# Kernel optimization log

Hardware: AMD Instinct MI355X
Metric: run time of the kernel (lower is better)

The kernel has to match this reference:

```python
import jax, jax.numpy as jnp
import numpy as np

B, D_IN, D_OUT = 16384, 1024, 1024


def setup_inputs() -> dict:
    key = jax.random.key(0)
    ks = jax.random.split(key, 14)
    s_x = 1.0 / np.sqrt(D_IN)
    s_h = 1.0 / np.sqrt(D_OUT)
    inp = {
        "inputs": jax.random.normal(ks[0], (B, D_IN), dtype=jnp.float32),
        "hist": jax.random.normal(ks[1], (B, D_OUT), dtype=jnp.float32),
        "carousel": 1,
    }
    names = ["f", "i", "o", "c"]
    for g, n in enumerate(names):
        inp[f"W{n}x"] = jax.random.normal(ks[2 + 3 * g], (D_IN, D_OUT), dtype=jnp.float32) * s_x
        inp[f"W{n}h"] = jax.random.normal(ks[3 + 3 * g], (D_OUT, D_OUT), dtype=jnp.float32) * s_h
        inp[f"b{n}"] = jnp.zeros((D_OUT,), dtype=jnp.float32)
    return inp


def reference(inputs, hist, carousel, Wfx, Wfh, bf, Wix, Wih, bi, Wox, Woh, bo, Wcx, Wch, bc):
    # Each GateMirrored: act(x @ Wx + h @ Wh + b)
    def gate(Wx, Wh, b, act):
        return act(inputs @ Wx + hist @ Wh + b)

    f = gate(Wfx, Wfh, bf, jax.nn.sigmoid)
    i = gate(Wix, Wih, bi, jax.nn.sigmoid)
    o = gate(Wox, Woh, bo, jax.nn.sigmoid)
    g = gate(Wcx, Wch, bc, jnp.tanh)

    c = f * jnp.float32(carousel) + i * g
    h = o * c
    return (h, c)
```

## Files before the change

### kernel.cpp

```cpp
#include <hip/hip_runtime.h>
#include <stdint.h>
#include <stddef.h>

#define B_ROWS 16384
#define DIN 1024
#define DOUT 1024
#define KDIM 2048

#define BM 256
#define BNP 256
#define BK 64

typedef __bf16 bf16x8 __attribute__((ext_vector_type(8)));
typedef float floatx4 __attribute__((ext_vector_type(4)));

__device__ __forceinline__ unsigned short f2bf(float f) {
  unsigned int u = __float_as_uint(f);
  u += 0x7fffu + ((u >> 16) & 1u);
  return (unsigned short)(u >> 16);
}

__device__ __forceinline__ void async16(const void* g, void* l) {
  __builtin_amdgcn_global_load_lds(
      (__attribute__((address_space(1))) void*)(g),
      (__attribute__((address_space(3))) void*)(l), 16, 0, 0);
}

__device__ __forceinline__ float sigmoid_f(float x) {
  return 1.0f / (1.0f + __expf(-x));
}
__device__ __forceinline__ float tanh_f(float x) {
  return 2.0f / (1.0f + __expf(-2.0f * x)) - 1.0f;
}

__global__ void prep_kernel(
    const float* __restrict__ inp, const float* __restrict__ hist,
    const float* __restrict__ s0, const float* __restrict__ s1,
    const float* __restrict__ s2, const float* __restrict__ s3,
    const float* __restrict__ s4, const float* __restrict__ s5,
    const float* __restrict__ s6, const float* __restrict__ s7,
    unsigned short* __restrict__ xb, unsigned short* __restrict__ wt) {
  __shared__ float tile[32][33];
  const int tid = threadIdx.x;
  if (blockIdx.x < 32768) {
    int idx = blockIdx.x * 256 + tid;
    const int per = B_ROWS * DIN / 4;
    const float* src;
    int colOff;
    int i = idx;
    if (i < per) { src = inp; colOff = 0; }
    else         { src = hist; colOff = DIN; i -= per; }
    int e = i * 4;
    int row = e >> 10;
    int col = e & 1023;
    const float4 v = *(const float4*)(src + (size_t)row * 1024 + col);
    ushort4 o;
    o.x = f2bf(v.x); o.y = f2bf(v.y); o.z = f2bf(v.z); o.w = f2bf(v.w);
    *(ushort4*)(xb + (size_t)row * KDIM + colOff + col) = o;
    return;
  }
  const int bb = blockIdx.x - 32768;
  const int bx = bb & 31, by = (bb >> 5) & 31, z = bb >> 10;
  const float* src;
  switch (z) {
    case 0: src = s0; break; case 1: src = s1; break;
    case 2: src = s2; break; case 3: src = s3; break;
    case 4: src = s4; break; case 5: src = s5; break;
    case 6: src = s6; break; default: src = s7; break;
  }
  const int g = z >> 1, part = z & 1;
  const int tx = tid & 31, ty = tid >> 5;
  const int n0 = bx * 32, k0 = by * 32;
#pragma unroll
  for (int j = 0; j < 32; j += 8)
    tile[ty + j][tx] = src[(size_t)(k0 + ty + j) * DOUT + n0 + tx];
  __syncthreads();
#pragma unroll
  for (int j = 0; j < 32; j += 8) {
    const int n = n0 + ty + j;
    const int np = ((n >> 4) << 6) + g * 16 + (n & 15);
    wt[(size_t)np * KDIM + part * DIN + k0 + tx] = f2bf(tile[tx][ty + j]);
  }
}

#define FENCE() __builtin_amdgcn_sched_barrier(0)
#define BAR() do { FENCE(); __builtin_amdgcn_s_barrier(); FENCE(); } while (0)
#define WAITV(N) asm volatile("s_waitcnt vmcnt(" #N ")" ::: "memory")
#define REGOFF(BUF, KH) (((BUF) * 2 + (KH)) << 13)

#define STAGE_A(BUF, KH, KT) do {                                          \
    unsigned short* d_ = As + REGOFF(BUF, KH) + tid * 8;                   \
    async16(agA + (KT) + (KH) * 32, d_);                                   \
    async16(agA + 128 * KDIM + (KT) + (KH) * 32, d_ + 4096);               \
  } while (0)
#define STAGE_B(BUF, KH, KT) do {                                          \
    unsigned short* d_ = Bs + REGOFF(BUF, KH) + tid * 8;                   \
    async16(agB + (KT) + (KH) * 32, d_);                                   \
    async16(agB + 128 * KDIM + (KT) + (KH) * 32, d_ + 4096);               \
  } while (0)
#define LDA4(BUF, KK, MH) do {                                             \
    const unsigned short* b_ = As + REGOFF(BUF, KK) + (MH) * 2048 + aoff;  \
    _Pragma("unroll")                                                      \
    for (int mi = 0; mi < 4; ++mi)                                         \
      av[mi] = *(const bf16x8*)(b_ + mi * 512);                            \
  } while (0)
#define LDB4(BUF, KK) do {                                                 \
    const unsigned short* b_ = Bs + REGOFF(BUF, KK) + boff;                \
    _Pragma("unroll")                                                      \
    for (int ni = 0; ni < 4; ++ni)                                         \
      bv[ni] = *(const bf16x8*)(b_ + ni * 512);                            \
  } while (0)
#define MFMA16(MH) do {                                                    \
    __builtin_amdgcn_s_setprio(1);                                         \
    _Pragma("unroll")                                                      \
    for (int mi = 0; mi < 4; ++mi)                                         \
      _Pragma("unroll")                                                    \
      for (int ni = 0; ni < 4; ++ni)                                       \
        acc[(MH) * 4 + mi][ni] = __builtin_amdgcn_mfma_f32_16x16x32_bf16(  \
            av[mi], bv[ni], acc[(MH) * 4 + mi][ni], 0, 0, 0);              \
    __builtin_amdgcn_s_setprio(0);                                         \
  } while (0)

__global__ __launch_bounds__(512, 2) void lstm_fused_kernel(
    const unsigned short* __restrict__ Xb,
    const unsigned short* __restrict__ Wt2,
    const float* __restrict__ b_f, const float* __restrict__ b_i,
    const float* __restrict__ b_o, const float* __restrict__ b_c,
    const int* __restrict__ carousel,
    float* __restrict__ out) {
  __shared__ unsigned short As[4 * 256 * 32];
  __shared__ unsigned short Bs[4 * 256 * 32];

  const int tid  = threadIdx.x;
  const int lane = tid & 63;
  const int wave = tid >> 6;
  const int wr   = wave >> 2;
  const int wc   = wave & 3;
  const int m16  = lane & 15;
  const int quad = lane >> 4;
  const int ua   = quad ^ ((m16 >> 1) & 3);
  const int bm   = blockIdx.y * BM;
  const int cg   = blockIdx.x;

  const unsigned short* Wp = Wt2 + (size_t)cg * BNP * KDIM;

  const int col = cg * 64 + wc * 16 + m16;
  const float bfv = b_f[col], biv = b_i[col], bov = b_o[col], bcv = b_c[col];
  const float cf  = (float)carousel[0];
  FENCE();

  const int srow   = tid >> 2;
  const int schunk = (tid & 3) ^ ((srow >> 1) & 3);
  const unsigned short* agA = Xb + (size_t)(bm + srow) * KDIM + schunk * 8;
  const unsigned short* agB = Wp + (size_t)srow * KDIM + schunk * 8;

  const int aoff = (wr * 128 + m16) * 32 + ua * 8;
  const int boff = (wc * 64 + m16) * 32 + ua * 8;

  floatx4 acc[8][4];
#pragma unroll
  for (int mi = 0; mi < 8; ++mi)
#pragma unroll
    for (int ni = 0; ni < 4; ++ni)
      acc[mi][ni] = (floatx4){0.f, 0.f, 0.f, 0.f};

  bf16x8 av[4], bv[4];

  STAGE_B(0, 0, 0);
  STAGE_A(0, 0, 0);
  STAGE_B(0, 1, 0);
  STAGE_A(0, 1, 0);
  STAGE_B(1, 0, 64);
  STAGE_A(1, 0, 64);
  STAGE_B(1, 1, 64);
  WAITV(10);
  BAR();

#pragma unroll 1
  for (int p = 0; p < 15; ++p) {
    const int kt = p * 128;
    LDA4(0, 0, 0); LDB4(0, 0);
    STAGE_A(1, 1, kt + 64);
    BAR(); MFMA16(0); BAR();
    LDA4(0, 0, 1);
    STAGE_B(0, 0, kt + 128);
    WAITV(10); BAR(); MFMA16(1); BAR();
    LDA4(0, 1, 0); LDB4(0, 1);
    STAGE_A(0, 0, kt + 128);
    BAR(); MFMA16(0); BAR();
    LDA4(0, 1, 1);
    STAGE_B(0, 1, kt + 128);
    WAITV(10); BAR(); MFMA16(1); BAR();
    LDA4(1, 0, 0); LDB4(1, 0);
    STAGE_A(0, 1, kt + 128);
    BAR(); MFMA16(0); BAR();
    LDA4(1, 0, 1);
    STAGE_B(1, 0, kt + 192);
    WAITV(10); BAR(); MFMA16(1); BAR();
    LDA4(1, 1, 0); LDB4(1, 1);
    STAGE_A(1, 0, kt + 192);
    BAR(); MFMA16(0); BAR();
    LDA4(1, 1, 1);
    STAGE_B(1, 1, kt + 192);
    WAITV(10); BAR(); MFMA16(1); BAR();
  }

  LDA4(0, 0, 0); LDB4(0, 0);
  STAGE_A(1, 1, 1984);
  BAR(); MFMA16(0); BAR();
  LDA4(0, 0, 1);
  WAITV(8); BAR(); MFMA16(1); BAR();
  LDA4(0, 1, 0); LDB4(0, 1);
  BAR(); MFMA16(0); BAR();
  LDA4(0, 1, 1);
  WAITV(4); BAR(); MFMA16(1); BAR();
  LDA4(1, 0, 0); LDB4(1, 0);
  BAR(); MFMA16(0); BAR();
  LDA4(1, 0, 1);
  WAITV(0); BAR(); MFMA16(1); BAR();
  LDA4(1, 1, 0); LDB4(1, 1);
  MFMA16(0);
  LDA4(1, 1, 1);
  MFMA16(1);

  const int rbase = bm + wr * 128 + quad * 4;
#pragma unroll
  for (int mi = 0; mi < 8; ++mi) {
#pragma unroll
    for (int r = 0; r < 4; ++r) {
      const int row = rbase + mi * 16 + r;
      const float f = sigmoid_f(acc[mi][0][r] + bfv);
      const float i = sigmoid_f(acc[mi][1][r] + biv);
      const float o = sigmoid_f(acc[mi][2][r] + bov);
      const float g = tanh_f   (acc[mi][3][r] + bcv);
      const float c = f * cf + i * g;
      const float h = o * c;
      out[(size_t)row * DOUT + col] = h;
      out[(size_t)(B_ROWS * DOUT) + (size_t)row * DOUT + col] = c;
    }
  }
}

extern "C" void kernel_launch(void* const* d_in, const int* in_sizes, int n_in,
                              void* d_out, int out_size, void* d_ws, size_t ws_size,
                              hipStream_t stream) {
  const float* inputs = (const float*)d_in[0];
  const float* hist   = (const float*)d_in[1];
  const int* carousel = (const int*)d_in[2];
  const float* Wfx = (const float*)d_in[3];
  const float* Wfh = (const float*)d_in[4];
  const float* bfv = (const float*)d_in[5];
  const float* Wix = (const float*)d_in[6];
  const float* Wih = (const float*)d_in[7];
  const float* biv = (const float*)d_in[8];
  const float* Wox = (const float*)d_in[9];
  const float* Woh = (const float*)d_in[10];
  const float* bov = (const float*)d_in[11];
  const float* Wcx = (const float*)d_in[12];
  const float* Wch = (const float*)d_in[13];
  const float* bcv = (const float*)d_in[14];

  unsigned short* Xb  = (unsigned short*)d_ws;
  unsigned short* Wt2 = Xb + (size_t)B_ROWS * KDIM;

  prep_kernel<<<40960, 256, 0, stream>>>(
      inputs, hist, Wfx, Wfh, Wix, Wih, Wox, Woh, Wcx, Wch, Xb, Wt2);

  dim3 grid(16, B_ROWS / BM);
  lstm_fused_kernel<<<grid, 512, 0, stream>>>(
      Xb, Wt2, bfv, biv, bov, bcv, carousel, (float*)d_out);
}
```

Baseline: 520.6 us.

## Restructure GEMM main loop to load full A fragment and issue 32 MFMAs per barrier phase

The main loop now stages A and B tiles together in one macro and loads all eight A fragments per k-half instead of splitting each k-half into two half-M phases. Each k-half issues 32 MFMAs between a single pair of barriers, halving the barrier count. Global pointers are advanced incrementally rather than recomputed from the loop index. The cost is more VGPRs for the A fragments, which may pressure the two-blocks-per-CU occupancy target, and less interleaving of LDS reads with MFMA work.

```diff
diff --git a/kernel.cpp b/kernel.cpp
--- a/kernel.cpp
+++ b/kernel.cpp
@@ -88,37 +88,36 @@
 #define WAITV(N) asm volatile("s_waitcnt vmcnt(" #N ")" ::: "memory")
 #define REGOFF(BUF, KH) (((BUF) * 2 + (KH)) << 13)
 
-#define STAGE_A(BUF, KH, KT) do {                                          \
-    unsigned short* d_ = As + REGOFF(BUF, KH) + tid * 8;                   \
-    async16(agA + (KT) + (KH) * 32, d_);                                   \
-    async16(agA + 128 * KDIM + (KT) + (KH) * 32, d_ + 4096);               \
-  } while (0)
-#define STAGE_B(BUF, KH, KT) do {                                          \
-    unsigned short* d_ = Bs + REGOFF(BUF, KH) + tid * 8;                   \
-    async16(agB + (KT) + (KH) * 32, d_);                                   \
-    async16(agB + 128 * KDIM + (KT) + (KH) * 32, d_ + 4096);               \
-  } while (0)
-#define LDA4(BUF, KK, MH) do {                                             \
-    const unsigned short* b_ = As + REGOFF(BUF, KK) + (MH) * 2048 + aoff;  \
-    _Pragma("unroll")                                                      \
-    for (int mi = 0; mi < 4; ++mi)                                         \
-      av[mi] = *(const bf16x8*)(b_ + mi * 512);                            \
-  } while (0)
-#define LDB4(BUF, KK) do {                                                 \
-    const unsigned short* b_ = Bs + REGOFF(BUF, KK) + boff;                \
-    _Pragma("unroll")                                                      \
-    for (int ni = 0; ni < 4; ++ni)                                         \
-      bv[ni] = *(const bf16x8*)(b_ + ni * 512);                            \
-  } while (0)
-#define MFMA16(MH) do {                                                    \
-    __builtin_amdgcn_s_setprio(1);                                         \
-    _Pragma("unroll")                                                      \
-    for (int mi = 0; mi < 4; ++mi)                                         \
-      _Pragma("unroll")                                                    \
-      for (int ni = 0; ni < 4; ++ni)                                       \
-        acc[(MH) * 4 + mi][ni] = __builtin_amdgcn_mfma_f32_16x16x32_bf16(  \
-            av[mi], bv[ni], acc[(MH) * 4 + mi][ni], 0, 0, 0);              \
-    __builtin_amdgcn_s_setprio(0);                                         \
+#define STAGE(BUF, KH, OFFE) do {                                           \
+    unsigned short* dA_ = As + REGOFF(BUF, KH) + tid * 8;                   \
+    unsigned short* dB_ = Bs + REGOFF(BUF, KH) + tid * 8;                   \
+    async16(pA0 + (OFFE), dA_);                                             \
+    async16(pA1 + (OFFE), dA_ + 4096);                                      \
+    async16(pB0 + (OFFE), dB_);                                             \
+    async16(pB1 + (OFFE), dB_ + 4096);                                      \
+  } while (0)
+
+#define LDB4(BUF, KK) do {                                                  \
+    const unsigned short* b_ = Bs + REGOFF(BUF, KK) + boff;                 \
+    _Pragma("unroll")                                                       \
+    for (int ni = 0; ni < 4; ++ni)                                          \
+      bv[ni] = *(const bf16x8*)(b_ + ni * 512);                             \
+  } while (0)
+#define LDA8(BUF, KK) do {                                                  \
+    const unsigned short* a_ = As + REGOFF(BUF, KK) + aoff;                 \
+    _Pragma("unroll")                                                       \
+    for (int mi = 0; mi < 8; ++mi)                                          \
+      av[mi] = *(const bf16x8*)(a_ + mi * 512);                             \
+  } while (0)
+#define MFMA32() do {                                                       \
+    __builtin_amdgcn_s_setprio(1);                                          \
+    _Pragma("unroll")                                                       \
+    for (int mi = 0; mi < 8; ++mi)                                          \
+      _Pragma("unroll")                                                     \
+      for (int ni = 0; ni < 4; ++ni)                                        \
+        acc[mi][ni] = __builtin_amdgcn_mfma_f32_16x16x32_bf16(              \
+            av[mi], bv[ni], acc[mi][ni], 0, 0, 0);                          \
+    __builtin_amdgcn_s_setprio(0);                                          \
   } while (0)
 
 __global__ __launch_bounds__(512, 2) void lstm_fused_kernel(
@@ -151,8 +150,10 @@
 
   const int srow   = tid >> 2;
   const int schunk = (tid & 3) ^ ((srow >> 1) & 3);
-  const unsigned short* agA = Xb + (size_t)(bm + srow) * KDIM + schunk * 8;
-  const unsigned short* agB = Wp + (size_t)srow * KDIM + schunk * 8;
+  const unsigned short* pA0 = Xb + (size_t)(bm + srow) * KDIM + schunk * 8;
+  const unsigned short* pA1 = pA0 + (size_t)128 * KDIM;
+  const unsigned short* pB0 = Wp + (size_t)srow * KDIM + schunk * 8;
+  const unsigned short* pB1 = pB0 + (size_t)128 * KDIM;
 
   const int aoff = (wr * 128 + m16) * 32 + ua * 8;
   const int boff = (wc * 64 + m16) * 32 + ua * 8;
@@ -164,64 +165,54 @@
     for (int ni = 0; ni < 4; ++ni)
       acc[mi][ni] = (floatx4){0.f, 0.f, 0.f, 0.f};
 
-  bf16x8 av[4], bv[4];
-
-  STAGE_B(0, 0, 0);
-  STAGE_A(0, 0, 0);
-  STAGE_B(0, 1, 0);
-  STAGE_A(0, 1, 0);
-  STAGE_B(1, 0, 64);
-  STAGE_A(1, 0, 64);
-  STAGE_B(1, 1, 64);
-  WAITV(10);
+  bf16x8 av[8], bv[4];
+
+  STAGE(0, 0, 0);
+  STAGE(0, 1, 32);
+  STAGE(1, 0, 64);
+  WAITV(8);
   BAR();
 
 #pragma unroll 1
   for (int p = 0; p < 15; ++p) {
-    const int kt = p * 128;
-    LDA4(0, 0, 0); LDB4(0, 0);
-    STAGE_A(1, 1, kt + 64);
-    BAR(); MFMA16(0); BAR();
-    LDA4(0, 0, 1);
-    STAGE_B(0, 0, kt + 128);
-    WAITV(10); BAR(); MFMA16(1); BAR();
-    LDA4(0, 1, 0); LDB4(0, 1);
-    STAGE_A(0, 0, kt + 128);
-    BAR(); MFMA16(0); BAR();
-    LDA4(0, 1, 1);
-    STAGE_B(0, 1, kt + 128);
-    WAITV(10); BAR(); MFMA16(1); BAR();
-    LDA4(1, 0, 0); LDB4(1, 0);
-    STAGE_A(0, 1, kt + 128);
-    BAR(); MFMA16(0); BAR();
-    LDA4(1, 0, 1);
-    STAGE_B(1, 0, kt + 192);
-    WAITV(10); BAR(); MFMA16(1); BAR();
-    LDA4(1, 1, 0); LDB4(1, 1);
-    STAGE_A(1, 0, kt + 192);
-    BAR(); MFMA16(0); BAR();
-    LDA4(1, 1, 1);
-    STAGE_B(1, 1, kt + 192);
-    WAITV(10); BAR(); MFMA16(1); BAR();
-  }
-
-  LDA4(0, 0, 0); LDB4(0, 0);
-  STAGE_A(1, 1, 1984);
-  BAR(); MFMA16(0); BAR();
-  LDA4(0, 0, 1);
-  WAITV(8); BAR(); MFMA16(1); BAR();
-  LDA4(0, 1, 0); LDB4(0, 1);
-  BAR(); MFMA16(0); BAR();
-  LDA4(0, 1, 1);
-  WAITV(4); BAR(); MFMA16(1); BAR();
-  LDA4(1, 0, 0); LDB4(1, 0);
-  BAR(); MFMA16(0); BAR();
-  LDA4(1, 0, 1);
-  WAITV(0); BAR(); MFMA16(1); BAR();
-  LDA4(1, 1, 0); LDB4(1, 1);
-  MFMA16(0);
-  LDA4(1, 1, 1);
-  MFMA16(1);
+    LDB4(0, 0); LDA8(0, 0);
+    STAGE(1, 1, 96);
+    WAITV(8); BAR();
+    MFMA32();
+    BAR();
+    LDB4(0, 1); LDA8(0, 1);
+    STAGE(0, 0, 128);
+    WAITV(8); BAR();
+    MFMA32();
+    BAR();
+    LDB4(1, 0); LDA8(1, 0);
+    STAGE(0, 1, 160);
+    WAITV(8); BAR();
+    MFMA32();
+    BAR();
+    LDB4(1, 1); LDA8(1, 1);
+    STAGE(1, 0, 192);
+    WAITV(8); BAR();
+    MFMA32();
+    BAR();
+    pA0 += 128; pA1 += 128; pB0 += 128; pB1 += 128;
+  }
+
+  LDB4(0, 0); LDA8(0, 0);
+  STAGE(1, 1, 96);
+  WAITV(8); BAR();
+  MFMA32();
+  BAR();
+  LDB4(0, 1); LDA8(0, 1);
+  WAITV(4); BAR();
+  MFMA32();
+  BAR();
+  LDB4(1, 0); LDA8(1, 0);
+  WAITV(0); BAR();
+  MFMA32();
+  BAR();
+  LDB4(1, 1); LDA8(1, 1);
+  MFMA32();
 
   const int rbase = bm + wr * 128 + quad * 4;
 #pragma unroll
```

Result: slower. 538.8 us (+3.5%).
